# Kernel tuning notes

Hardware: AMD Instinct MI355X
Metric: run time of the kernel (lower is better)

The kernel has to match this reference:

```python
import jax, jax.numpy as jnp
import numpy as np
import math

B, C, IMG, E, H, L, FF, D, NCLS = 4, 3, 64, 256, 8, 512, 4, 4, 1000
N = IMG * IMG  # 4096 pixel tokens
HS = H * E    # head_size = embedding_size * heads (per original code)


def setup_inputs() -> dict:
    key = jax.random.key(0)
    ks = jax.random.split(key, 32)
    s = 0.02
    nrm = lambda k, shape: (jax.random.normal(k, shape, jnp.float32) * s)
    inp = {
        "x": jax.random.normal(ks[0], (B, C, N), jnp.float32),
        "conv_w": nrm(ks[1], (E, C)),                 # 1x1 conv1d kernel
        "conv_b": jnp.zeros((E,), jnp.float32),
        "pos_emb": nrm(ks[2], (N, E)),
        "latents": jax.random.normal(ks[3], (L, E), jnp.float32),
        # cross-attention (queries from latents, keys/values from image tokens)
        "ca_wq": nrm(ks[4], (E, HS)),
        "ca_wk": nrm(ks[5], (E, HS)),
        "ca_wv": nrm(ks[6], (E, HS)),
        "ca_wu": nrm(ks[7], (HS, E)),
        "ca_bu": jnp.zeros((E,), jnp.float32),
        "ca_ln_g": jnp.ones((E,), jnp.float32),
        "ca_ln_b": jnp.zeros((E,), jnp.float32),
        # transformer blocks, stacked along depth for lax.scan
        "blk_wq": nrm(ks[8], (D, E, HS)),
        "blk_wk": nrm(ks[9], (D, E, HS)),
        "blk_wv": nrm(ks[10], (D, E, HS)),
        "blk_wu": nrm(ks[11], (D, HS, E)),
        "blk_bu": jnp.zeros((D, E), jnp.float32),
        "blk_ln1_g": jnp.ones((D, E), jnp.float32),
        "blk_ln1_b": jnp.zeros((D, E), jnp.float32),
        "blk_w1": nrm(ks[12], (D, E, FF * E)),
        "blk_b1": jnp.zeros((D, FF * E), jnp.float32),
        "blk_w2": nrm(ks[13], (D, FF * E, E)),
        "blk_b2": jnp.zeros((D, E), jnp.float32),
        "blk_ln2_g": jnp.ones((D, E), jnp.float32),
        "blk_ln2_b": jnp.zeros((D, E), jnp.float32),
        "cls_w": nrm(ks[14], (E, NCLS)),
        "cls_b": jnp.zeros((NCLS,), jnp.float32),
        "heads": H,
    }
    return inp


def _ln(x, g, b):
    m = jnp.mean(x, axis=-1, keepdims=True)
    v = jnp.mean(jnp.square(x - m), axis=-1, keepdims=True)
    return g * (x - m) * jax.lax.rsqrt(v + 1e-5) + b


def _mha(q_in, kv_in, wq, wk, wv, wu, bu, heads):
    # Faithful to original: each head has dim = embedding_size (head_size = heads*emb),
    # and the scale is sqrt(emb // heads).
    b, nq, e = q_in.shape
    nk = kv_in.shape[1]
    q = (q_in @ wq).reshape(b, nq, heads, e)
    k = (kv_in @ wk).reshape(b, nk, heads, e)
    v = (kv_in @ wv).reshape(b, nk, heads, e)
    scale = 1.0 / math.sqrt(e // heads)
    w = jax.nn.softmax(jnp.einsum('bqhe,bkhe->bhqk', q, k) * scale, axis=-1)
    a = jnp.einsum('bhqk,bkhe->bqhe', w, v).reshape(b, nq, heads * e)
    return a @ wu + bu


def reference(x, conv_w, conv_b, pos_emb, latents,
              ca_wq, ca_wk, ca_wv, ca_wu, ca_bu, ca_ln_g, ca_ln_b,
              blk_wq, blk_wk, blk_wv, blk_wu, blk_bu,
              blk_ln1_g, blk_ln1_b, blk_w1, blk_b1, blk_w2, blk_b2,
              blk_ln2_g, blk_ln2_b, cls_w, cls_b, heads):
    bsz = x.shape[0]
    # 1x1 conv1d over flattened pixels: (B, C, N) -> (B, N, E), plus positions
    tokens = jnp.einsum('bcn,ec->bne', x, conv_w) + conv_b + pos_emb
    # latents as queries, image tokens as keys/values (cross-attention)
    z = jnp.broadcast_to(latents, (bsz,) + latents.shape)
    z = _ln(_mha(z, tokens, ca_wq, ca_wk, ca_wv, ca_wu, ca_bu, heads) + z,
            ca_ln_g, ca_ln_b)
    # dropout is identity in eval mode

    def block(z, p):
        wq, wk, wv, wu, bu, g1, b1, w1, c1, w2, c2, g2, b2 = p
        z = _ln(_mha(z, z, wq, wk, wv, wu, bu, heads) + z, g1, b1)
        h = jax.nn.gelu(z @ w1 + c1, approximate=False) @ w2 + c2
        z = _ln(h + z, g2, b2)
        return z, None

    z, _ = jax.lax.scan(block, z,
                        (blk_wq, blk_wk, blk_wv, blk_wu, blk_bu,
                         blk_ln1_g, blk_ln1_b, blk_w1, blk_b1,
                         blk_w2, blk_b2, blk_ln2_g, blk_ln2_b))
    # global average over latents, then classifier
    return jnp.mean(z, axis=1) @ cls_w + cls_b
```

## Files before the change

### kernel.cpp

```cpp
#include <hip/hip_runtime.h>
#include <hip/hip_bf16.h>
#include <math.h>


typedef __attribute__((ext_vector_type(8))) short s8v;
typedef __attribute__((ext_vector_type(4))) float f32x4;

__device__ __forceinline__ short f2b(float f) {
  union { float f; unsigned u; } a; a.f = f;
  unsigned r = a.u + 0x7fff + ((a.u >> 16) & 1);
  return (short)(r >> 16);
}
__device__ __forceinline__ float b2f(short s) {
  union { unsigned u; float f; } a; a.u = ((unsigned)(unsigned short)s) << 16;
  return a.f;
}

__device__ __forceinline__ void gl16(const void* gp, void* lp) {
  __builtin_amdgcn_global_load_lds(
      (const __attribute__((address_space(1))) unsigned int*)gp,
      (__attribute__((address_space(3))) unsigned int*)lp, 16, 0, 0);
}

__global__ __launch_bounds__(256) void k_tokens(
    const float* __restrict__ x, const float* __restrict__ cw,
    const float* __restrict__ cb, const float* __restrict__ pe,
    short* __restrict__ tok)
{
  int idx = blockIdx.x * 256 + threadIdx.x;
  int e = idx & 255;
  int n = (idx >> 8) & 4095;
  int b = idx >> 20;
  float s = cb[e] + pe[n * 256 + e];
#pragma unroll
  for (int c = 0; c < 3; ++c)
    s += x[b * 12288 + c * 4096 + n] * cw[e * 3 + c];
  tok[idx] = f2b(s);
}

template<typename TI>
__global__ __launch_bounds__(256) void k_tr(
    const TI* __restrict__ in, short* __restrict__ out,
    int R, int C, long sIn, long sOut)
{
  __shared__ float t[32][33];
  const TI* ib = in + (long)blockIdx.z * sIn;
  short* ob = out + (long)blockIdx.z * sOut;
  int c0 = blockIdx.x * 32, r0 = blockIdx.y * 32;
  int tx = threadIdx.x & 31, ty = threadIdx.x >> 5;
#pragma unroll
  for (int i = 0; i < 4; ++i)
    t[ty * 4 + i][tx] = (float)ib[(long)(r0 + ty * 4 + i) * C + c0 + tx];
  __syncthreads();
#pragma unroll
  for (int i = 0; i < 4; ++i)
    ob[(long)(c0 + ty * 4 + i) * R + r0 + tx] = f2b(t[tx][ty * 4 + i]);
}

struct TrJob {
  const float* src; short* dst;
  int R, C; long sIn, sOut;
  int mode, tilesPerZ, z, tileBase;
};
struct TrJobs { TrJob j[11]; };

__global__ __launch_bounds__(256) void k_trbatch(TrJobs jb, int njobs)
{
  __shared__ float t[32][33];
  int tb = blockIdx.x, ji = 0;
#pragma unroll
  for (int k = 1; k < 11; ++k)
    if (k < njobs && tb >= jb.j[k].tileBase) ji = k;
  TrJob J = jb.j[ji];
  int local = tb - J.tileBase;
  if (J.mode == 1) {
    long o = (long)local * 8192 + threadIdx.x;
#pragma unroll
    for (int k = 0; k < 32; ++k) J.dst[o + k * 256] = f2b(J.src[o + k * 256]);
    return;
  }
  int zi = local / J.tilesPerZ, ti = local - zi * J.tilesPerZ;
  int ntx = J.C >> 5;
  int tx = ti % ntx, ty = ti / ntx;
  const float* ib = J.src + (long)zi * J.sIn;
  short* ob = J.dst + (long)zi * J.sOut;
  int c0 = tx * 32, r0 = ty * 32;
  int lx = threadIdx.x & 31, ly = threadIdx.x >> 5;
#pragma unroll
  for (int i = 0; i < 4; ++i)
    t[ly * 4 + i][lx] = ib[(long)(r0 + ly * 4 + i) * J.C + c0 + lx];
  __syncthreads();
#pragma unroll
  for (int i = 0; i < 4; ++i)
    ob[(long)(c0 + ly * 4 + i) * J.R + r0 + lx] = f2b(t[lx][ly * 4 + i]);
}

template<int EPI>
__global__ __launch_bounds__(256) void k_mgemm(
    const short* __restrict__ A, const short* __restrict__ Bt,
    void* __restrict__ Cv, const float* __restrict__ bias,
    int K, int lda, int ldb, int ldc,
    long sA, long sB, long sC, int zdA, int zmA, int zdB, int zmB)
{
  __shared__ char As[8192];
  __shared__ char Bs[8192];
  int z = blockIdx.z;
  const short* Ab = A + ((long)((z / zdA) % zmA)) * sA;
  const short* Bb = Bt + ((long)((z / zdB) % zmB)) * sB;
  int t = threadIdx.x;
  int lane = t & 63, w = t >> 6;
  int wr = w >> 1, wc = w & 1;
  int g = lane >> 4, l15 = lane & 15;
  long row0 = (long)blockIdx.y * 128, col0 = (long)blockIdx.x * 128;
  const f32x4 zz = {0.f, 0.f, 0.f, 0.f};
  f32x4 acc[4][4];
#pragma unroll
  for (int m = 0; m < 4; ++m)
#pragma unroll
    for (int n = 0; n < 4; ++n) acc[m][n] = zz;

  auto mload = [&](s8v* aa, s8v* bb, int kk) {
#pragma unroll
    for (int i = 0; i < 2; ++i) {
      int r = i * 64 + (t >> 2), c = t & 3;
      aa[i] = *(const s8v*)&Ab[(row0 + r) * (long)lda + kk + c * 8];
      bb[i] = *(const s8v*)&Bb[(col0 + r) * (long)ldb + kk + c * 8];
    }
  };
  auto mstore = [&](s8v* aa, s8v* bb) {
#pragma unroll
    for (int i = 0; i < 2; ++i) {
      int r = i * 64 + (t >> 2), c = t & 3;
      int off = (r * 64 + c * 16) ^ ((r & 7) << 4);
      *(s8v*)&As[off] = aa[i];
      *(s8v*)&Bs[off] = bb[i];
    }
  };
  auto mcomp = [&]() {
    s8v af[4], bfr[4];
#pragma unroll
    for (int m = 0; m < 4; ++m) {
      int r = wr * 64 + m * 16 + l15;
      af[m] = *(const s8v*)&As[(r * 64 + g * 16) ^ ((r & 7) << 4)];
    }
#pragma unroll
    for (int n = 0; n < 4; ++n) {
      int r = wc * 64 + n * 16 + l15;
      bfr[n] = *(const s8v*)&Bs[(r * 64 + g * 16) ^ ((r & 7) << 4)];
    }
#pragma unroll
    for (int m = 0; m < 4; ++m)
#pragma unroll
      for (int n = 0; n < 4; ++n)
        acc[m][n] = __builtin_amdgcn_mfma_f32_16x16x32_bf16(af[m], bfr[n], acc[m][n], 0, 0, 0);
  };

  s8v a0[2], b0[2], a1[2], b1[2];
  mload(a0, b0, 0);
  for (int k0 = 0; k0 < K; k0 += 64) {
    __syncthreads(); mstore(a0, b0); __syncthreads();
    mload(a1, b1, k0 + 32);
    mcomp();
    __syncthreads(); mstore(a1, b1); __syncthreads();
    if (k0 + 64 < K) mload(a0, b0, k0 + 64);
    mcomp();
  }

  long zo = (long)z * sC;
#pragma unroll
  for (int m = 0; m < 4; ++m)
#pragma unroll
    for (int n = 0; n < 4; ++n)
#pragma unroll
      for (int r = 0; r < 4; ++r) {
        long rr = row0 + wr * 64 + m * 16 + g * 4 + r;
        long cc = col0 + wc * 64 + n * 16 + l15;
        float v = acc[m][n][r];
        if (EPI == 1) {
          v += bias[cc];
          v = 0.5f * v * (1.f + erff(v * 0.70710678118654752f));
        }
        if (EPI == 2)
          ((float*)Cv)[zo + rr * ldc + cc] = v;
        else
          ((short*)Cv)[zo + rr * ldc + cc] = f2b(v);
      }
}

__global__ __launch_bounds__(512, 2) void k_mflash4(
    const short* __restrict__ Qp, const short* __restrict__ Kp,
    const short* __restrict__ Vtp, short* __restrict__ Opart,
    float* __restrict__ MLp,
    int nk, int ldq, int ldk, int ldvt,
    long qh, long qb, long kh, long kb, long vh, long vb, float scale)
{
  __shared__ char pool[81920];
  int t = threadIdx.x, lane = t & 63, w = t >> 6;
  int g = lane >> 4, l15 = lane & 15;
  int h = blockIdx.y, b = blockIdx.z;
  int kv = blockIdx.x & 3, qblk = blockIdx.x >> 2;
  const short* Q  = Qp  + (long)h * qh + (long)b * qb;
  const short* Kg = Kp  + (long)h * kh + (long)b * kb;
  const short* Vg = Vtp + (long)h * vh + (long)b * vb;
  char* Pw = pool + 65536 + w * 2048;
  int q0 = qblk * 256 + w * 32;
  int nkq = nk >> 2;
  int NIT = nkq >> 5;
  int k0base = kv * nkq;

  s8v qf[2][8];
#pragma unroll
  for (int s = 0; s < 2; ++s) {
    const short* Qrow = Q + (long)(q0 + s * 16 + l15) * ldq + g * 8;
#pragma unroll
    for (int ks = 0; ks < 8; ++ks) qf[s][ks] = *(const s8v*)(Qrow + ks * 32);
  }

  int krow0 = w * 2 + (lane >> 5);
  const char* kgRow = (const char*)(Kg + (long)(k0base + krow0) * ldk)
                      + (((lane & 31) ^ (krow0 & 7)) * 16);
  int vrow0 = w * 16 + (lane >> 2);
  const char* vgRow = (const char*)(Vg + (long)vrow0 * ldvt + k0base)
                      + (((lane & 3) ^ ((vrow0 >> 1) & 3)) * 16);
  const long kStep = (long)32 * ldk * 2;
  const long kCOff = (long)16 * ldk * 2;
  const long vCOff = (long)128 * ldvt * 2;

  auto stage = [&](int bsel) {
    char* base = pool + bsel * 32768;
#pragma unroll
    for (int c = 0; c < 2; ++c)
      gl16(kgRow + c * kCOff, base + c * 8192 + w * 1024);
#pragma unroll
    for (int c = 0; c < 2; ++c)
      gl16(vgRow + c * vCOff, base + 16384 + c * 8192 + w * 1024);
  };

  const f32x4 zz = {0.f, 0.f, 0.f, 0.f};
  f32x4 accO[2][16];
#pragma unroll
  for (int s = 0; s < 2; ++s)
#pragma unroll
    for (int i = 0; i < 16; ++i) accO[s][i] = zz;
  float mrow[2][4] = {{-1e30f, -1e30f, -1e30f, -1e30f},
                      {-1e30f, -1e30f, -1e30f, -1e30f}};
  float lrow[2][4] = {{0.f, 0.f, 0.f, 0.f}, {0.f, 0.f, 0.f, 0.f}};

  stage(0);
  kgRow += kStep; vgRow += 64;

  for (int it = 0; it < NIT; ++it) {
    int cur = it & 1;
    asm volatile("s_waitcnt vmcnt(0)" ::: "memory");
    __syncthreads();
    if (it + 1 < NIT) {
      stage(cur ^ 1);
      kgRow += kStep; vgRow += 64;
    }
    const char* kls = pool + cur * 32768;
    const char* vls = kls + 16384;

    f32x4 sacc[2][2];
    __builtin_amdgcn_s_setprio(1);
#pragma unroll
    for (int kc = 0; kc < 2; ++kc) {
      sacc[0][kc] = zz; sacc[1][kc] = zz;
#pragma unroll
      for (int ks = 0; ks < 8; ++ks) {
        s8v bfr = *(const s8v*)&kls[(kc * 16 + l15) * 512 + (((ks * 4 + g) ^ (l15 & 7)) * 16)];
        sacc[0][kc] = __builtin_amdgcn_mfma_f32_16x16x32_bf16(qf[0][ks], bfr, sacc[0][kc], 0, 0, 0);
        sacc[1][kc] = __builtin_amdgcn_mfma_f32_16x16x32_bf16(qf[1][ks], bfr, sacc[1][kc], 0, 0, 0);
      }
    }
    __builtin_amdgcn_s_setprio(0);

#pragma unroll
    for (int s = 0; s < 2; ++s) {
#pragma unroll
      for (int kc = 0; kc < 2; ++kc)
#pragma unroll
        for (int r = 0; r < 4; ++r) sacc[s][kc][r] *= scale;
      float mt[4];
#pragma unroll
      for (int r = 0; r < 4; ++r) mt[r] = fmaxf(sacc[s][0][r], sacc[s][1][r]);
#pragma unroll
      for (int o = 1; o < 16; o <<= 1)
#pragma unroll
        for (int r = 0; r < 4; ++r) mt[r] = fmaxf(mt[r], __shfl_xor(mt[r], o));
      float dmax = fmaxf(fmaxf(mt[0] - mrow[s][0], mt[1] - mrow[s][1]),
                         fmaxf(mt[2] - mrow[s][2], mt[3] - mrow[s][3]));
      if (__any(dmax > 8.f)) {
#pragma unroll
        for (int r = 0; r < 4; ++r) {
          float mn = fmaxf(mrow[s][r], mt[r]);
          float al = __expf(mrow[s][r] - mn);
          mrow[s][r] = mn; lrow[s][r] *= al;
#pragma unroll
          for (int n = 0; n < 16; ++n) accO[s][n][r] *= al;
        }
      }
      float lsum[4] = {0.f, 0.f, 0.f, 0.f};
#pragma unroll
      for (int kc = 0; kc < 2; ++kc)
#pragma unroll
        for (int r = 0; r < 4; ++r) {
          float p = __expf(sacc[s][kc][r] - mrow[s][r]);
          lsum[r] += p;
          *(short*)&Pw[s * 1024 + (g * 4 + r) * 64 + ((kc * 32 + l15 * 2) ^ (g << 4))] = f2b(p);
        }
#pragma unroll
      for (int o = 1; o < 16; o <<= 1)
#pragma unroll
        for (int r = 0; r < 4; ++r) lsum[r] += __shfl_xor(lsum[r], o);
#pragma unroll
      for (int r = 0; r < 4; ++r) lrow[s][r] += lsum[r];
    }
    s8v pa0 = *(const s8v*)&Pw[l15 * 64 + ((g * 16) ^ ((l15 >> 2) << 4))];
    s8v pa1 = *(const s8v*)&Pw[1024 + l15 * 64 + ((g * 16) ^ ((l15 >> 2) << 4))];

    __builtin_amdgcn_s_setprio(1);
#pragma unroll
    for (int n = 0; n < 16; ++n) {
      s8v vf = *(const s8v*)&vls[(n * 16 + l15) * 64 + ((g ^ ((l15 >> 1) & 3)) * 16)];
      accO[0][n] = __builtin_amdgcn_mfma_f32_16x16x32_bf16(pa0, vf, accO[0][n], 0, 0, 0);
      accO[1][n] = __builtin_amdgcn_mfma_f32_16x16x32_bf16(pa1, vf, accO[1][n], 0, 0, 0);
    }
    __builtin_amdgcn_s_setprio(0);
  }

  long prow = (((long)kv * 4 + b) * 8 + h) * 512;
  short* Ob = Opart + prow * 256;
  float* MLb = MLp + prow * 2;
#pragma unroll
  for (int s = 0; s < 2; ++s) {
    if (l15 == 0) {
#pragma unroll
      for (int r = 0; r < 4; ++r) {
        int row = q0 + s * 16 + g * 4 + r;
        MLb[row * 2] = mrow[s][r];
        MLb[row * 2 + 1] = lrow[s][r];
      }
    }
#pragma unroll
    for (int n = 0; n < 16; ++n)
#pragma unroll
      for (int r = 0; r < 4; ++r)
        Ob[(long)(q0 + s * 16 + g * 4 + r) * 256 + n * 16 + l15] = f2b(accO[s][n][r]);
  }
}

__global__ __launch_bounds__(512) void k_fcomb(
    const short* __restrict__ Op, const float* __restrict__ ML,
    short* __restrict__ O)
{
  int d = threadIdx.x & 255;
  int q = blockIdx.x * 2 + (threadIdx.x >> 8);
  int h = blockIdx.y, b = blockIdx.z;
  const long kvs = 4L * 8 * 512;
  long r0 = ((long)b * 8 + h) * 512 + q;
  float mm[4], ll[4], m = -1e30f;
#pragma unroll
  for (int kv = 0; kv < 4; ++kv) {
    mm[kv] = ML[(kv * kvs + r0) * 2];
    ll[kv] = ML[(kv * kvs + r0) * 2 + 1];
    m = fmaxf(m, mm[kv]);
  }
  float wv[4], lsum = 0.f;
#pragma unroll
  for (int kv = 0; kv < 4; ++kv) { wv[kv] = __expf(mm[kv] - m); lsum += ll[kv] * wv[kv]; }
  float inv = 1.f / lsum, acc = 0.f;
#pragma unroll
  for (int kv = 0; kv < 4; ++kv)
    acc += b2f(Op[(kv * kvs + r0) * 256 + d]) * wv[kv];
  O[(long)b * 1048576 + (long)q * 2048 + h * 256 + d] = f2b(acc * inv);
}

__global__ __launch_bounds__(256) void k_bias_res_ln(
    const float* __restrict__ Yp, int nPart, long pStride,
    const float* __restrict__ bias,
    const float* __restrict__ res, int resMod,
    const float* __restrict__ g, const float* __restrict__ bta,
    float* __restrict__ out, short* __restrict__ out_bf)
{
  __shared__ float red[4];
  int row = blockIdx.x, e = threadIdx.x;
  float v = bias[e] + res[(long)(row % resMod) * 256 + e];
  for (int s = 0; s < nPart; ++s) v += Yp[s * pStride + (long)row * 256 + e];
  float s1 = v;
#pragma unroll
  for (int o = 32; o > 0; o >>= 1) s1 += __shfl_down(s1, o);
  if ((e & 63) == 0) red[e >> 6] = s1;
  __syncthreads();
  float mean = (red[0] + red[1] + red[2] + red[3]) * (1.f / 256.f);
  float d = v - mean;
  __syncthreads();
  float s2 = d * d;
#pragma unroll
  for (int o = 32; o > 0; o >>= 1) s2 += __shfl_down(s2, o);
  if ((e & 63) == 0) red[e >> 6] = s2;
  __syncthreads();
  float var = (red[0] + red[1] + red[2] + red[3]) * (1.f / 256.f);
  float o = g[e] * d * rsqrtf(var + 1e-5f) + bta[e];
  out[(long)row * 256 + e] = o;
  out_bf[(long)row * 256 + e] = f2b(o);
}

__global__ __launch_bounds__(256) void k_meancls(
    const float* __restrict__ z, const float* __restrict__ w,
    const float* __restrict__ bias, float* __restrict__ out)
{
  __shared__ float zms[256];
  int b = blockIdx.y, e = threadIdx.x;
  float s = 0.f;
  for (int l = 0; l < 512; ++l) s += z[((long)b * 512 + l) * 256 + e];
  zms[e] = s * (1.f / 512.f);
  __syncthreads();
  int j = blockIdx.x * 256 + e;
  if (j >= 1000) return;
  float acc = bias[j];
  for (int e2 = 0; e2 < 256; ++e2) acc += zms[e2] * w[e2 * 1000 + j];
  out[b * 1000 + j] = acc;
}

extern "C" void kernel_launch(void* const* d_in, const int* in_sizes, int n_in,
                              void* d_out, int out_size, void* d_ws, size_t ws_size,
                              hipStream_t stream)
{
  (void)in_sizes; (void)n_in; (void)out_size; (void)ws_size;
  const float* x       = (const float*)d_in[0];
  const float* conv_w  = (const float*)d_in[1];
  const float* conv_b  = (const float*)d_in[2];
  const float* pos_emb = (const float*)d_in[3];
  const float* latents = (const float*)d_in[4];
  const float* ca_wq   = (const float*)d_in[5];
  const float* ca_wk   = (const float*)d_in[6];
  const float* ca_wv   = (const float*)d_in[7];
  const float* ca_wu   = (const float*)d_in[8];
  const float* ca_bu   = (const float*)d_in[9];
  const float* ca_ln_g = (const float*)d_in[10];
  const float* ca_ln_b = (const float*)d_in[11];
  const float* blk_wq  = (const float*)d_in[12];
  const float* blk_wk  = (const float*)d_in[13];
  const float* blk_wv  = (const float*)d_in[14];
  const float* blk_wu  = (const float*)d_in[15];
  const float* blk_bu  = (const float*)d_in[16];
  const float* blk_ln1_g = (const float*)d_in[17];
  const float* blk_ln1_b = (const float*)d_in[18];
  const float* blk_w1  = (const float*)d_in[19];
  const float* blk_b1  = (const float*)d_in[20];
  const float* blk_w2  = (const float*)d_in[21];
  const float* blk_b2  = (const float*)d_in[22];
  const float* blk_ln2_g = (const float*)d_in[23];
  const float* blk_ln2_b = (const float*)d_in[24];
  const float* cls_w   = (const float*)d_in[25];
  const float* cls_b   = (const float*)d_in[26];
  float* out = (float*)d_out;

  short* wqT_ca = (short*)d_ws;
  short* wkT_ca = wqT_ca + 524288;
  short* wuT_ca = wkT_ca + 524288;
  short* wv_ca  = wuT_ca + 524288;
  short* lat_bf = wv_ca + 524288;
  short* wqkT   = lat_bf + 131072;
  short* wvT    = wqkT + 4194304;
  short* wuT_b  = wvT + 2097152;
  short* w1T    = wuT_b + 2097152;
  short* w2T    = w1T + 1048576;
  short* tok_bf = w2T + 1048576;
  short* tokT   = tok_bf + 4194304;
  short* qCA    = tokT + 4194304;
  short* qtil   = qCA + 1048576;
  short* MstT   = qtil + 1048576;
  short* VtB    = MstT + 524288;
  short* bufO   = VtB + 4194304;
  short* h1     = bufO + 4194304;
  short* z_bf   = h1 + 2097152;
  float* z      = (float*)(z_bf + 524288);
  float* zm     = z + 524288;
  float* Ypart  = zm + 1024;
  short* Opart  = (short*)(Ypart + 4194304);
  float* MLp    = (float*)(Opart + 16777216);
  short* QKb    = tok_bf;

  const float scale = 0.17677669529663687f;
  const int BIG = 1 << 30;

  TrJobs JB; int nj = 0, base = 0;
  auto addT = [&](const float* s, short* d, int R, int C, long sIn, long sOut, int zc) {
    int tpz = (C >> 5) * (R >> 5);
    JB.j[nj] = {s, d, R, C, sIn, sOut, 0, tpz, zc, base};
    base += tpz * zc; ++nj;
  };
  auto addC = [&](const float* s, short* d, int nelem) {
    int tpz = nelem >> 13;
    JB.j[nj] = {s, d, 0, 0, 0, 0, 1, tpz, 1, base};
    base += tpz; ++nj;
  };
  addT(ca_wq, wqT_ca, 256, 2048, 0, 0, 1);
  addT(ca_wk, wkT_ca, 256, 2048, 0, 0, 1);
  addT(ca_wu, wuT_ca, 2048, 256, 0, 0, 1);
  addT(blk_wq, wqkT, 256, 2048, 524288, 1048576, 4);
  addT(blk_wk, wqkT + 524288, 256, 2048, 524288, 1048576, 4);
  addT(blk_wv, wvT, 256, 2048, 524288, 524288, 4);
  addT(blk_wu, wuT_b, 2048, 256, 524288, 524288, 4);
  addT(blk_w1, w1T, 256, 1024, 262144, 262144, 4);
  addT(blk_w2, w2T, 1024, 256, 262144, 262144, 4);
  addC(ca_wv, wv_ca, 524288);
  addC(latents, lat_bf, 131072);
  k_trbatch<<<base, 256, 0, stream>>>(JB, nj);

  k_tokens<<<16384, 256, 0, stream>>>(x, conv_w, conv_b, pos_emb, tok_bf);
  k_tr<__hip_bfloat16><<<dim3(8, 128, 4), 256, 0, stream>>>(
      (const __hip_bfloat16*)tok_bf, tokT, 4096, 256, 1048576, 1048576);

  k_mgemm<0><<<dim3(16, 4, 1), 256, 0, stream>>>(
      lat_bf, wqT_ca, qCA, nullptr, 256, 256, 256, 2048, 0, 0, 0, 1, BIG, 1, BIG);
  k_mgemm<0><<<dim3(2, 4, 8), 256, 0, stream>>>(
      qCA, wkT_ca, qtil, nullptr, 256, 2048, 256, 256, 256, 65536, 131072, 1, 8, 1, 8);
  k_mgemm<0><<<dim3(2, 2, 8), 256, 0, stream>>>(
      wuT_ca, wv_ca, MstT, nullptr, 256, 2048, 2048, 2048, 256, 256, 256, 1, 8, 1, 8);
  k_mflash4<<<dim3(8, 8, 4), 512, 0, stream>>>(
      qtil, tok_bf, tokT, Opart, MLp, 4096, 256, 256, 4096,
      131072L, 0L, 0L, 1048576L, 0L, 1048576L, scale);
  k_fcomb<<<dim3(256, 8, 4), 512, 0, stream>>>(Opart, MLp, bufO);
  k_mgemm<2><<<dim3(2, 16, 8), 256, 0, stream>>>(
      bufO, MstT, Ypart, nullptr, 256, 2048, 2048, 256, 256, 256, 524288, 1, 8, 1, 8);
  k_bias_res_ln<<<2048, 256, 0, stream>>>(Ypart, 8, 524288L, ca_bu, latents, 512,
                                          ca_ln_g, ca_ln_b, z, z_bf);

  for (int d = 0; d < 4; ++d) {
    k_mgemm<0><<<dim3(32, 16, 1), 256, 0, stream>>>(
        z_bf, wqkT + (long)d * 1048576, QKb, nullptr,
        256, 256, 256, 4096, 0, 0, 0, 1, BIG, 1, BIG);
    k_mgemm<0><<<dim3(4, 2, 32), 256, 0, stream>>>(
        wvT + (long)d * 524288, z_bf, VtB, nullptr,
        256, 256, 256, 512, 65536, 131072, 131072, 1, 8, 8, BIG);
    k_mflash4<<<dim3(8, 8, 4), 512, 0, stream>>>(
        QKb, QKb + 2048, VtB, Opart, MLp, 512, 4096, 4096, 512,
        256L, 2097152L, 256L, 2097152L, 131072L, 1048576L, scale);
    k_fcomb<<<dim3(256, 8, 4), 512, 0, stream>>>(Opart, MLp, bufO);
    k_mgemm<2><<<dim3(2, 16, 8), 256, 0, stream>>>(
        bufO, wuT_b + (long)d * 524288, Ypart, nullptr,
        256, 2048, 2048, 256, 256, 256, 524288, 1, 8, 1, 8);
    k_bias_res_ln<<<2048, 256, 0, stream>>>(Ypart, 8, 524288L, blk_bu + d * 256, z, 2048,
        blk_ln1_g + d * 256, blk_ln1_b + d * 256, z, z_bf);
    k_mgemm<1><<<dim3(8, 16, 1), 256, 0, stream>>>(
        z_bf, w1T + (long)d * 262144, h1, blk_b1 + d * 1024,
        256, 256, 256, 1024, 0, 0, 0, 1, BIG, 1, BIG);
    k_mgemm<2><<<dim3(2, 16, 8), 256, 0, stream>>>(
        h1, w2T + (long)d * 262144, Ypart, nullptr,
        128, 1024, 1024, 256, 128, 128, 524288, 1, 8, 1, 8);
    k_bias_res_ln<<<2048, 256, 0, stream>>>(Ypart, 8, 524288L, blk_b2 + d * 256, z, 2048,
        blk_ln2_g + d * 256, blk_ln2_b + d * 256, z, z_bf);
  }

  k_meancls<<<dim3(4, 4), 256, 0, stream>>>(z, cls_w, cls_b, out);
}
```

Measured before the change: 655.3 us.

## Rewrite flash attention with 32x32 MFMA, register P, and prescaled Q weights

The flash-attention kernel now uses 32x32x16 bf16 MFMA tiles with 64-key iterations and a larger double-buffered LDS pool. Q is used as the B operand, so each lane holds one query row and the softmax row reductions become in-register. P is packed to bf16 with cvt_pk and moved into the A-operand layout with lane shuffles instead of a round trip through LDS. The softmax scale is folded into the Q weight conversion, so the per-iteration multiply goes away. The cost is a 128KB LDS footprint that may limit occupancy, plus higher register pressure.

```diff
diff --git a/kernel.cpp b/kernel.cpp
--- a/kernel.cpp
+++ b/kernel.cpp
@@ -5,6 +5,8 @@
 
 typedef __attribute__((ext_vector_type(8))) short s8v;
 typedef __attribute__((ext_vector_type(4))) float f32x4;
+typedef __attribute__((ext_vector_type(16))) float f32x16;
+typedef __attribute__((ext_vector_type(4))) unsigned u32x4;
 
 __device__ __forceinline__ short f2b(float f) {
   union { float f; unsigned u; } a; a.f = f;
@@ -14,6 +16,11 @@
 __device__ __forceinline__ float b2f(short s) {
   union { unsigned u; float f; } a; a.u = ((unsigned)(unsigned short)s) << 16;
   return a.f;
+}
+__device__ __forceinline__ unsigned cvtpk(float lo, float hi) {
+  unsigned r;
+  asm("v_cvt_pk_bf16_f32 %0, %1, %2" : "=v"(r) : "v"(lo), "v"(hi));
+  return r;
 }
 
 __device__ __forceinline__ void gl16(const void* gp, void* lp) {
@@ -61,6 +68,7 @@
   const float* src; short* dst;
   int R, C; long sIn, sOut;
   int mode, tilesPerZ, z, tileBase;
+  float scale;
 };
 struct TrJobs { TrJob j[11]; };
 
@@ -76,7 +84,8 @@
   if (J.mode == 1) {
     long o = (long)local * 8192 + threadIdx.x;
 #pragma unroll
-    for (int k = 0; k < 32; ++k) J.dst[o + k * 256] = f2b(J.src[o + k * 256]);
+    for (int k = 0; k < 32; ++k)
+      J.dst[o + k * 256] = f2b(J.src[o + k * 256] * J.scale);
     return;
   }
   int zi = local / J.tilesPerZ, ti = local - zi * J.tilesPerZ;
@@ -92,7 +101,7 @@
   __syncthreads();
 #pragma unroll
   for (int i = 0; i < 4; ++i)
-    ob[(long)(c0 + ly * 4 + i) * J.R + r0 + lx] = f2b(t[lx][ly * 4 + i]);
+    ob[(long)(c0 + ly * 4 + i) * J.R + r0 + lx] = f2b(t[lx][ly * 4 + i] * J.scale);
 }
 
 template<int EPI>
@@ -187,143 +196,143 @@
       }
 }
 
-__global__ __launch_bounds__(512, 2) void k_mflash4(
+__global__ __launch_bounds__(512, 2) void k_mflash5(
     const short* __restrict__ Qp, const short* __restrict__ Kp,
     const short* __restrict__ Vtp, short* __restrict__ Opart,
     float* __restrict__ MLp,
     int nk, int ldq, int ldk, int ldvt,
-    long qh, long qb, long kh, long kb, long vh, long vb, float scale)
-{
-  __shared__ char pool[81920];
+    long qh, long qb, long kh, long kb, long vh, long vb)
+{
+  __shared__ char pool[131072];
   int t = threadIdx.x, lane = t & 63, w = t >> 6;
-  int g = lane >> 4, l15 = lane & 15;
+  int l31 = lane & 31, hi = lane >> 5;
   int h = blockIdx.y, b = blockIdx.z;
   int kv = blockIdx.x & 3, qblk = blockIdx.x >> 2;
   const short* Q  = Qp  + (long)h * qh + (long)b * qb;
   const short* Kg = Kp  + (long)h * kh + (long)b * kb;
   const short* Vg = Vtp + (long)h * vh + (long)b * vb;
-  char* Pw = pool + 65536 + w * 2048;
-  int q0 = qblk * 256 + w * 32;
+  int q0w = qblk * 256 + w * 32;
   int nkq = nk >> 2;
-  int NIT = nkq >> 5;
-  int k0base = kv * nkq;
-
-  s8v qf[2][8];
-#pragma unroll
-  for (int s = 0; s < 2; ++s) {
-    const short* Qrow = Q + (long)(q0 + s * 16 + l15) * ldq + g * 8;
-#pragma unroll
-    for (int ks = 0; ks < 8; ++ks) qf[s][ks] = *(const s8v*)(Qrow + ks * 32);
-  }
-
-  int krow0 = w * 2 + (lane >> 5);
-  const char* kgRow = (const char*)(Kg + (long)(k0base + krow0) * ldk)
-                      + (((lane & 31) ^ (krow0 & 7)) * 16);
-  int vrow0 = w * 16 + (lane >> 2);
-  const char* vgRow = (const char*)(Vg + (long)vrow0 * ldvt + k0base)
-                      + (((lane & 3) ^ ((vrow0 >> 1) & 3)) * 16);
-  const long kStep = (long)32 * ldk * 2;
-  const long kCOff = (long)16 * ldk * 2;
-  const long vCOff = (long)128 * ldvt * 2;
+  int NIT = nkq >> 6;
+  long k0 = (long)kv * nkq;
+
+  s8v qf[16];
+  {
+    const short* Qrow = Q + (long)(q0w + l31) * ldq + hi * 8;
+#pragma unroll
+    for (int s = 0; s < 16; ++s) qf[s] = *(const s8v*)(Qrow + s * 16);
+  }
+
+  const char* KgB = (const char*)Kg;
+  const char* VgB = (const char*)Vg;
+  unsigned koff[4], voff[4];
+#pragma unroll
+  for (int c = 0; c < 4; ++c) {
+    int r = 8 * w + 2 * c + hi;
+    koff[c] = (unsigned)((k0 + r) * (long)ldk * 2) + ((l31 ^ (r & 31)) << 4);
+    int rv = 32 * w + 8 * c + (lane >> 3);
+    voff[c] = (unsigned)(((long)rv * ldvt + k0) * 2) + (((lane & 7) ^ (lane >> 3)) << 4);
+  }
+  const unsigned kStep = (unsigned)(64 * ldk * 2);
 
   auto stage = [&](int bsel) {
-    char* base = pool + bsel * 32768;
-#pragma unroll
-    for (int c = 0; c < 2; ++c)
-      gl16(kgRow + c * kCOff, base + c * 8192 + w * 1024);
-#pragma unroll
-    for (int c = 0; c < 2; ++c)
-      gl16(vgRow + c * vCOff, base + 16384 + c * 8192 + w * 1024);
+    char* kd = pool + bsel * 65536 + (w << 12);
+    char* vd = kd + 32768;
+#pragma unroll
+    for (int c = 0; c < 4; ++c) { gl16(KgB + koff[c], kd + c * 1024); koff[c] += kStep; }
+#pragma unroll
+    for (int c = 0; c < 4; ++c) { gl16(VgB + voff[c], vd + c * 1024); voff[c] += 128; }
   };
 
-  const f32x4 zz = {0.f, 0.f, 0.f, 0.f};
-  f32x4 accO[2][16];
-#pragma unroll
-  for (int s = 0; s < 2; ++s)
-#pragma unroll
-    for (int i = 0; i < 16; ++i) accO[s][i] = zz;
-  float mrow[2][4] = {{-1e30f, -1e30f, -1e30f, -1e30f},
-                      {-1e30f, -1e30f, -1e30f, -1e30f}};
-  float lrow[2][4] = {{0.f, 0.f, 0.f, 0.f}, {0.f, 0.f, 0.f, 0.f}};
+  f32x16 accO[8];
+#pragma unroll
+  for (int n = 0; n < 8; ++n)
+#pragma unroll
+    for (int i = 0; i < 16; ++i) accO[n][i] = 0.f;
+  float mrow = -1e30f, lrow = 0.f;
 
   stage(0);
-  kgRow += kStep; vgRow += 64;
 
   for (int it = 0; it < NIT; ++it) {
     int cur = it & 1;
     asm volatile("s_waitcnt vmcnt(0)" ::: "memory");
     __syncthreads();
-    if (it + 1 < NIT) {
-      stage(cur ^ 1);
-      kgRow += kStep; vgRow += 64;
-    }
-    const char* kls = pool + cur * 32768;
-    const char* vls = kls + 16384;
-
-    f32x4 sacc[2][2];
+    if (it + 1 < NIT) stage(cur ^ 1);
+    const char* kls = pool + cur * 65536;
+    const char* vls = kls + 32768;
+
+    f32x16 sacc[2];
+#pragma unroll
+    for (int i = 0; i < 16; ++i) { sacc[0][i] = 0.f; sacc[1][i] = 0.f; }
     __builtin_amdgcn_s_setprio(1);
 #pragma unroll
-    for (int kc = 0; kc < 2; ++kc) {
-      sacc[0][kc] = zz; sacc[1][kc] = zz;
-#pragma unroll
-      for (int ks = 0; ks < 8; ++ks) {
-        s8v bfr = *(const s8v*)&kls[(kc * 16 + l15) * 512 + (((ks * 4 + g) ^ (l15 & 7)) * 16)];
-        sacc[0][kc] = __builtin_amdgcn_mfma_f32_16x16x32_bf16(qf[0][ks], bfr, sacc[0][kc], 0, 0, 0);
-        sacc[1][kc] = __builtin_amdgcn_mfma_f32_16x16x32_bf16(qf[1][ks], bfr, sacc[1][kc], 0, 0, 0);
+    for (int tt = 0; tt < 2; ++tt) {
+      int r = tt * 32 + l31;
+#pragma unroll
+      for (int s = 0; s < 16; ++s) {
+        s8v kf = *(const s8v*)&kls[r * 512 + (((2 * s + hi) ^ l31) << 4)];
+        sacc[tt] = __builtin_amdgcn_mfma_f32_32x32x16_bf16(kf, qf[s], sacc[tt], 0, 0, 0);
       }
     }
     __builtin_amdgcn_s_setprio(0);
 
-#pragma unroll
-    for (int s = 0; s < 2; ++s) {
-#pragma unroll
-      for (int kc = 0; kc < 2; ++kc)
-#pragma unroll
-        for (int r = 0; r < 4; ++r) sacc[s][kc][r] *= scale;
-      float mt[4];
-#pragma unroll
-      for (int r = 0; r < 4; ++r) mt[r] = fmaxf(sacc[s][0][r], sacc[s][1][r]);
-#pragma unroll
-      for (int o = 1; o < 16; o <<= 1)
-#pragma unroll
-        for (int r = 0; r < 4; ++r) mt[r] = fmaxf(mt[r], __shfl_xor(mt[r], o));
-      float dmax = fmaxf(fmaxf(mt[0] - mrow[s][0], mt[1] - mrow[s][1]),
-                         fmaxf(mt[2] - mrow[s][2], mt[3] - mrow[s][3]));
-      if (__any(dmax > 8.f)) {
-#pragma unroll
-        for (int r = 0; r < 4; ++r) {
-          float mn = fmaxf(mrow[s][r], mt[r]);
-          float al = __expf(mrow[s][r] - mn);
-          mrow[s][r] = mn; lrow[s][r] *= al;
-#pragma unroll
-          for (int n = 0; n < 16; ++n) accO[s][n][r] *= al;
-        }
+    float mt = sacc[0][0];
+#pragma unroll
+    for (int i = 1; i < 16; ++i) mt = fmaxf(mt, sacc[0][i]);
+#pragma unroll
+    for (int i = 0; i < 16; ++i) mt = fmaxf(mt, sacc[1][i]);
+    mt = fmaxf(mt, __shfl_xor(mt, 32));
+    if (__any(mt - mrow > 8.f)) {
+      float mn = fmaxf(mrow, mt);
+      float al = __expf(mrow - mn);
+      mrow = mn; lrow *= al;
+#pragma unroll
+      for (int r = 0; r < 16; ++r) {
+        float alr = __shfl(al, (r & 3) + 8 * (r >> 2) + 4 * hi);
+#pragma unroll
+        for (int n = 0; n < 8; ++n) accO[n][r] *= alr;
       }
-      float lsum[4] = {0.f, 0.f, 0.f, 0.f};
-#pragma unroll
-      for (int kc = 0; kc < 2; ++kc)
-#pragma unroll
-        for (int r = 0; r < 4; ++r) {
-          float p = __expf(sacc[s][kc][r] - mrow[s][r]);
-          lsum[r] += p;
-          *(short*)&Pw[s * 1024 + (g * 4 + r) * 64 + ((kc * 32 + l15 * 2) ^ (g << 4))] = f2b(p);
-        }
-#pragma unroll
-      for (int o = 1; o < 16; o <<= 1)
-#pragma unroll
-        for (int r = 0; r < 4; ++r) lsum[r] += __shfl_xor(lsum[r], o);
-#pragma unroll
-      for (int r = 0; r < 4; ++r) lrow[s][r] += lsum[r];
-    }
-    s8v pa0 = *(const s8v*)&Pw[l15 * 64 + ((g * 16) ^ ((l15 >> 2) << 4))];
-    s8v pa1 = *(const s8v*)&Pw[1024 + l15 * 64 + ((g * 16) ^ ((l15 >> 2) << 4))];
+    }
+    float ls = 0.f;
+#pragma unroll
+    for (int tt = 0; tt < 2; ++tt)
+#pragma unroll
+      for (int i = 0; i < 16; ++i) {
+        float p = __expf(sacc[tt][i] - mrow);
+        sacc[tt][i] = p; ls += p;
+      }
+    ls += __shfl_xor(ls, 32);
+    lrow += ls;
+
+    s8v pa[4];
+#pragma unroll
+    for (int s = 0; s < 4; ++s) {
+      int tt = s >> 1, r0 = (s & 1) * 8;
+      unsigned w0 = cvtpk(sacc[tt][r0 + 0], sacc[tt][r0 + 1]);
+      unsigned w1 = cvtpk(sacc[tt][r0 + 2], sacc[tt][r0 + 3]);
+      unsigned w2 = cvtpk(sacc[tt][r0 + 4], sacc[tt][r0 + 5]);
+      unsigned w3 = cvtpk(sacc[tt][r0 + 6], sacc[tt][r0 + 7]);
+      unsigned x0 = (unsigned)__shfl_xor((int)w0, 32);
+      unsigned x1 = (unsigned)__shfl_xor((int)w1, 32);
+      unsigned x2 = (unsigned)__shfl_xor((int)w2, 32);
+      unsigned x3 = (unsigned)__shfl_xor((int)w3, 32);
+      u32x4 pw;
+      pw.x = hi ? x2 : w0;
+      pw.y = hi ? x3 : w1;
+      pw.z = hi ? w2 : x0;
+      pw.w = hi ? w3 : x1;
+      pa[s] = *(s8v*)&pw;
+    }
 
     __builtin_amdgcn_s_setprio(1);
 #pragma unroll
-    for (int n = 0; n < 16; ++n) {
-      s8v vf = *(const s8v*)&vls[(n * 16 + l15) * 64 + ((g ^ ((l15 >> 1) & 3)) * 16)];
-      accO[0][n] = __builtin_amdgcn_mfma_f32_16x16x32_bf16(pa0, vf, accO[0][n], 0, 0, 0);
-      accO[1][n] = __builtin_amdgcn_mfma_f32_16x16x32_bf16(pa1, vf, accO[1][n], 0, 0, 0);
+    for (int n = 0; n < 8; ++n) {
+      int rv = n * 32 + l31;
+#pragma unroll
+      for (int s2 = 0; s2 < 4; ++s2) {
+        s8v vf = *(const s8v*)&vls[rv * 128 + (((2 * s2 + hi) ^ (l31 & 7)) << 4)];
+        accO[n] = __builtin_amdgcn_mfma_f32_32x32x16_bf16(pa[s2], vf, accO[n], 0, 0, 0);
+      }
     }
     __builtin_amdgcn_s_setprio(0);
   }
@@ -331,22 +340,17 @@
   long prow = (((long)kv * 4 + b) * 8 + h) * 512;
   short* Ob = Opart + prow * 256;
   float* MLb = MLp + prow * 2;
-#pragma unroll
-  for (int s = 0; s < 2; ++s) {
-    if (l15 == 0) {
-#pragma unroll
-      for (int r = 0; r < 4; ++r) {
-        int row = q0 + s * 16 + g * 4 + r;
-        MLb[row * 2] = mrow[s][r];
-        MLb[row * 2 + 1] = lrow[s][r];
-      }
-    }
-#pragma unroll
-    for (int n = 0; n < 16; ++n)
-#pragma unroll
-      for (int r = 0; r < 4; ++r)
-        Ob[(long)(q0 + s * 16 + g * 4 + r) * 256 + n * 16 + l15] = f2b(accO[s][n][r]);
-  }
+  if (lane < 32) {
+    MLb[(q0w + l31) * 2] = mrow;
+    MLb[(q0w + l31) * 2 + 1] = lrow;
+  }
+#pragma unroll
+  for (int n = 0; n < 8; ++n)
+#pragma unroll
+    for (int r = 0; r < 16; ++r) {
+      int q = q0w + (r & 3) + 8 * (r >> 2) + 4 * hi;
+      Ob[(long)q * 256 + n * 32 + l31] = f2b(accO[n][r]);
+    }
 }
 
 __global__ __launch_bounds__(512) void k_fcomb(
@@ -486,25 +490,26 @@
   const int BIG = 1 << 30;
 
   TrJobs JB; int nj = 0, base = 0;
-  auto addT = [&](const float* s, short* d, int R, int C, long sIn, long sOut, int zc) {
+  auto addT = [&](const float* s, short* d, int R, int C, long sIn, long sOut,
+                  int zc, float sc) {
     int tpz = (C >> 5) * (R >> 5);
-    JB.j[nj] = {s, d, R, C, sIn, sOut, 0, tpz, zc, base};
+    JB.j[nj] = {s, d, R, C, sIn, sOut, 0, tpz, zc, base, sc};
     base += tpz * zc; ++nj;
   };
   auto addC = [&](const float* s, short* d, int nelem) {
     int tpz = nelem >> 13;
-    JB.j[nj] = {s, d, 0, 0, 0, 0, 1, tpz, 1, base};
+    JB.j[nj] = {s, d, 0, 0, 0, 0, 1, tpz, 1, base, 1.f};
     base += tpz; ++nj;
   };
-  addT(ca_wq, wqT_ca, 256, 2048, 0, 0, 1);
-  addT(ca_wk, wkT_ca, 256, 2048, 0, 0, 1);
-  addT(ca_wu, wuT_ca, 2048, 256, 0, 0, 1);
-  addT(blk_wq, wqkT, 256, 2048, 524288, 1048576, 4);
-  addT(blk_wk, wqkT + 524288, 256, 2048, 524288, 1048576, 4);
-  addT(blk_wv, wvT, 256, 2048, 524288, 524288, 4);
-  addT(blk_wu, wuT_b, 2048, 256, 524288, 524288, 4);
-  addT(blk_w1, w1T, 256, 1024, 262144, 262144, 4);
-  addT(blk_w2, w2T, 1024, 256, 262144, 262144, 4);
+  addT(ca_wq, wqT_ca, 256, 2048, 0, 0, 1, scale);
+  addT(ca_wk, wkT_ca, 256, 2048, 0, 0, 1, 1.f);
+  addT(ca_wu, wuT_ca, 2048, 256, 0, 0, 1, 1.f);
+  addT(blk_wq, wqkT, 256, 2048, 524288, 1048576, 4, scale);
+  addT(blk_wk, wqkT + 524288, 256, 2048, 524288, 1048576, 4, 1.f);
+  addT(blk_wv, wvT, 256, 2048, 524288, 524288, 4, 1.f);
+  addT(blk_wu, wuT_b, 2048, 256, 524288, 524288, 4, 1.f);
+  addT(blk_w1, w1T, 256, 1024, 262144, 262144, 4, 1.f);
+  addT(blk_w2, w2T, 1024, 256, 262144, 262144, 4, 1.f);
   addC(ca_wv, wv_ca, 524288);
   addC(latents, lat_bf, 131072);
   k_trbatch<<<base, 256, 0, stream>>>(JB, nj);
@@ -519,9 +524,9 @@
       qCA, wkT_ca, qtil, nullptr, 256, 2048, 256, 256, 256, 65536, 131072, 1, 8, 1, 8);
   k_mgemm<0><<<dim3(2, 2, 8), 256, 0, stream>>>(
       wuT_ca, wv_ca, MstT, nullptr, 256, 2048, 2048, 2048, 256, 256, 256, 1, 8, 1, 8);
-  k_mflash4<<<dim3(8, 8, 4), 512, 0, stream>>>(
+  k_mflash5<<<dim3(8, 8, 4), 512, 0, stream>>>(
       qtil, tok_bf, tokT, Opart, MLp, 4096, 256, 256, 4096,
-      131072L, 0L, 0L, 1048576L, 0L, 1048576L, scale);
+      131072L, 0L, 0L, 1048576L, 0L, 1048576L);
   k_fcomb<<<dim3(256, 8, 4), 512, 0, stream>>>(Opart, MLp, bufO);
   k_mgemm<2><<<dim3(2, 16, 8), 256, 0, stream>>>(
       bufO, MstT, Ypart, nullptr, 256, 2048, 2048, 256, 256, 256, 524288, 1, 8, 1, 8);
@@ -535,9 +540,9 @@
     k_mgemm<0><<<dim3(4, 2, 32), 256, 0, stream>>>(
         wvT + (long)d * 524288, z_bf, VtB, nullptr,
         256, 256, 256, 512, 65536, 131072, 131072, 1, 8, 8, BIG);
-    k_mflash4<<<dim3(8, 8, 4), 512, 0, stream>>>(
+    k_mflash5<<<dim3(8, 8, 4), 512, 0, stream>>>(
         QKb, QKb + 2048, VtB, Opart, MLp, 512, 4096, 4096, 512,
-        256L, 2097152L, 256L, 2097152L, 131072L, 1048576L, scale);
+        256L, 2097152L, 256L, 2097152L, 131072L, 1048576L);
     k_fcomb<<<dim3(256, 8, 4), 512, 0, stream>>>(Opart, MLp, bufO);
     k_mgemm<2><<<dim3(2, 16, 8), 256, 0, stream>>>(
         bufO, wuT_b + (long)d * 524288, Ypart, nullptr,
```

New measurement: 635.7 us. 3.0% less time.
